# Optimization experiments

Measured on AMD Instinct MI355X. Metric: run time of the kernel, lower is better.

The kernel has to match this reference:

```python
import jax, jax.numpy as jnp
import numpy as np

B, L, D, Y = 8, 2500, 512, 8921


def setup_inputs() -> dict:
    key = jax.random.key(0)
    k1, k2, k3, k4, k5, k6 = jax.random.split(key, 6)
    x = jax.random.normal(k1, (B, L, D), dtype=jnp.float32)
    target = jax.random.uniform(k2, (B, Y), dtype=jnp.float32)
    text_inputs = jax.random.randint(k3, (B, L), 0, 50000, dtype=jnp.int32)
    # Xavier-uniform-like init for the two [Y, D] weights
    lim = float(np.sqrt(6.0 / (Y + D)))
    U_weight = jax.random.uniform(k4, (Y, D), dtype=jnp.float32, minval=-lim, maxval=lim)
    final_weight = jax.random.uniform(k5, (Y, D), dtype=jnp.float32, minval=-lim, maxval=lim)
    final_bias = jax.random.uniform(k6, (Y,), dtype=jnp.float32, minval=-0.05, maxval=0.05)
    return {"x": x, "target": target, "text_inputs": text_inputs,
            "U_weight": U_weight, "final_weight": final_weight, "final_bias": final_bias}


def reference(x, target, text_inputs, U_weight, final_weight, final_bias):
    # att: [B, Y, L] = U.weight @ x^T
    att = jnp.einsum('yd,bld->byl', U_weight, x)
    # softmax over sequence dim
    alpha = jax.nn.softmax(att, axis=2)
    # per-label context: [B, Y, D]
    m = jnp.einsum('byl,bld->byd', alpha, x)
    # gated reduction instead of a linear layer: [B, Y]
    y = jnp.einsum('byd,yd->by', m, final_weight) + final_bias
    # BCEWithLogitsLoss (mean over all elements), numerically stable
    loss = jnp.mean(jnp.maximum(y, 0.0) - y * target + jnp.log1p(jnp.exp(-jnp.abs(y))))
    return (y, loss)
```

## Files before the change

### kernel.cpp

```cpp
#include <hip/hip_runtime.h>
#include <stdint.h>

#define B_ 8
#define L_ 2500
#define D_ 512
#define Y_ 8921
#define LP 2560
#define YP 8960
#define BY 128
#define BL 256
#define BK 32
#define NKT 16
#define NSP 10
#define NBLK (70 * B_ * NSP)
#define PERX (NBLK / 8)
#define BUF 16384

typedef float f32x4 __attribute__((ext_vector_type(4)));
typedef __bf16 bf16x8 __attribute__((ext_vector_type(8)));
typedef unsigned short u16;
typedef unsigned int u32;

__device__ __forceinline__ u32 pack2(float a, float b) {
  u32 ua = __float_as_uint(a); ua = (ua + 0x7FFFu + ((ua >> 16) & 1u)) >> 16;
  u32 ub = __float_as_uint(b); ub = (ub + 0x7FFFu + ((ub >> 16) & 1u)) >> 16;
  return ua | (ub << 16);
}

__global__ void cvt_x_kernel(const float* __restrict__ x, u16* __restrict__ xb) {
  int idx = blockIdx.x * 256 + threadIdx.x;
  int row = idx >> 6;
  int c8  = (idx & 63) << 3;
  int b = row / LP;
  int l = row - b * LP;
  uint4 o;
  if (l < L_) {
    const float* s = x + (size_t)(b * L_ + l) * D_ + c8;
    float4 f0 = *(const float4*)s;
    float4 f1 = *(const float4*)(s + 4);
    o.x = pack2(f0.x, f0.y); o.y = pack2(f0.z, f0.w);
    o.z = pack2(f1.x, f1.y); o.w = pack2(f1.z, f1.w);
  } else {
    o = make_uint4(0u, 0u, 0u, 0u);
  }
  *(uint4*)(xb + (size_t)row * D_ + c8) = o;
}

__global__ void cvt_w_kernel(const float* __restrict__ U, const float* __restrict__ Wf,
                             u16* __restrict__ Ub, u16* __restrict__ Wb) {
  int idx = blockIdx.x * 256 + threadIdx.x;
  const int half = YP * 64;
  const float* src = U; u16* dst = Ub;
  int i = idx;
  if (idx >= half) { i -= half; src = Wf; dst = Wb; }
  int row = i >> 6;
  int c8  = (i & 63) << 3;
  uint4 o;
  if (row < Y_) {
    const float* s = src + (size_t)row * D_ + c8;
    float4 f0 = *(const float4*)s;
    float4 f1 = *(const float4*)(s + 4);
    o.x = pack2(f0.x, f0.y); o.y = pack2(f0.z, f0.w);
    o.z = pack2(f1.x, f1.y); o.w = pack2(f1.z, f1.w);
  } else {
    o = make_uint4(0u, 0u, 0u, 0u);
  }
  *(uint4*)(dst + (size_t)row * D_ + c8) = o;
}

__device__ __forceinline__ void async16(const u16* g, u16* l) {
  __builtin_amdgcn_global_load_lds(
      (const __attribute__((address_space(1))) u32*)g,
      (__attribute__((address_space(3))) u32*)l, 16, 0, 0);
}

__global__ __launch_bounds__(512, 2) void fused_kernel(
    const u16* __restrict__ xb,
    const u16* __restrict__ Ub,
    const u16* __restrict__ Wb,
    float* __restrict__ part)
{
  __shared__ __align__(16) u16 sB[2 * BUF];
  __shared__ float sSt[3 * 4 * BY];

  const int t    = threadIdx.x;
  const int lane = t & 63;
  const int wv   = t >> 6;
  const int wy   = wv >> 2;
  const int wl   = wv & 3;
  const int l16  = lane & 15;
  const int q    = lane >> 4;

  const int bid = blockIdx.x;
  const int w   = (bid & 7) * PERX + (bid >> 3);
  const int yt  = w / 80;
  const int rem = w - yt * 80;
  const int b   = rem / NSP;
  const int s   = rem - b * NSP;
  const int y0  = yt * BY;
  const int l0  = s * BL;

  const int srow = t >> 2;
  const int scol = (t & 3) << 3;
  const u16* gU  = Ub + (size_t)(y0 + srow) * D_ + scol;
  const u16* gW  = Wb + (size_t)(y0 + srow) * D_ + scol;
  const u16* gX0 = xb + ((size_t)b * LP + l0 + srow) * D_ + scol;
  const u16* gX1 = gX0 + (size_t)128 * D_;

  const int offU = (wy * 64 + l16) * BK + q * 8;
  const int offX = 8192 + (wl * 64 + l16) * BK + q * 8;

  auto stage = [&](int kt, int buf) {
    u16* base = sB + buf * BUF;
    const int ko = kt * BK;
    async16(gU + ko,  base + t * 8);
    async16(gW + ko,  base + 4096 + t * 8);
    async16(gX0 + ko, base + 8192 + t * 8);
    async16(gX1 + ko, base + 12288 + t * 8);
  };

  const f32x4 z4 = {0.f, 0.f, 0.f, 0.f};
  f32x4 accA[4][4], accS[4][4];
#pragma unroll
  for (int yi = 0; yi < 4; ++yi)
#pragma unroll
    for (int xi = 0; xi < 4; ++xi) { accA[yi][xi] = z4; accS[yi][xi] = z4; }

  stage(0, 0);
#pragma unroll 1
  for (int kt = 0; kt < NKT; ++kt) {
    const int cur = kt & 1;
    if (kt + 1 < NKT) {
      stage(kt + 1, cur ^ 1);
      asm volatile("s_waitcnt vmcnt(4)" ::: "memory");
    } else {
      asm volatile("s_waitcnt vmcnt(0)" ::: "memory");
    }
    __builtin_amdgcn_s_barrier();
    asm volatile("" ::: "memory");

    const u16* bb = sB + cur * BUF;
    bf16x8 xf[4];
#pragma unroll
    for (int xi = 0; xi < 4; ++xi)
      xf[xi] = *(const bf16x8*)(const void*)(bb + offX + xi * 16 * BK);
    __builtin_amdgcn_s_setprio(1);
#pragma unroll
    for (int yi = 0; yi < 4; ++yi) {
      bf16x8 aU = *(const bf16x8*)(const void*)(bb + offU + yi * 16 * BK);
      bf16x8 aW = *(const bf16x8*)(const void*)(bb + 4096 + offU + yi * 16 * BK);
#pragma unroll
      for (int xi = 0; xi < 4; ++xi) {
        accA[yi][xi] = __builtin_amdgcn_mfma_f32_16x16x32_bf16(aU, xf[xi], accA[yi][xi], 0, 0, 0);
        accS[yi][xi] = __builtin_amdgcn_mfma_f32_16x16x32_bf16(aW, xf[xi], accS[yi][xi], 0, 0, 0);
      }
    }
    __builtin_amdgcn_s_setprio(0);
    asm volatile("" ::: "memory");
    __builtin_amdgcn_s_barrier();
  }

  float M[16], Z[16], W[16];
  const bool boundary = (l0 + BL > L_);
#pragma unroll
  for (int yi = 0; yi < 4; ++yi) {
#pragma unroll
    for (int r = 0; r < 4; ++r) {
      const int si = yi * 4 + r;
      float a[4];
#pragma unroll
      for (int xi = 0; xi < 4; ++xi) {
        float v = accA[yi][xi][r];
        a[xi] = (boundary && (l0 + wl * 64 + xi * 16 + l16 >= L_)) ? -1e30f : v;
      }
      const float mx = fmaxf(fmaxf(a[0], a[1]), fmaxf(a[2], a[3]));
      float zl = 0.f, wl_ = 0.f;
#pragma unroll
      for (int xi = 0; xi < 4; ++xi) {
        const float p = __expf(a[xi] - mx);
        zl += p;
        wl_ = fmaf(p, accS[yi][xi][r], wl_);
      }
      M[si] = mx; Z[si] = zl; W[si] = wl_;
    }
  }

#pragma unroll
  for (int si = 0; si < 16; ++si) {
    float M0 = M[si], Z0 = Z[si], W0 = W[si];
#pragma unroll
    for (int st = 1; st <= 8; st <<= 1) {
      const float Mo = __shfl_xor(M0, st);
      const float Zo = __shfl_xor(Z0, st);
      const float Wo = __shfl_xor(W0, st);
      const float mn = fmaxf(M0, Mo);
      const float sa = __expf(M0 - mn);
      const float sb = __expf(Mo - mn);
      Z0 = Z0 * sa + Zo * sb;
      W0 = W0 * sa + Wo * sb;
      M0 = mn;
    }
    M[si] = M0; Z[si] = Z0; W[si] = W0;
  }

  __syncthreads();
  if (l16 == 0) {
#pragma unroll
    for (int yi = 0; yi < 4; ++yi) {
#pragma unroll
      for (int r = 0; r < 4; ++r) {
        const int si = yi * 4 + r;
        const int yloc = wy * 64 + yi * 16 + q * 4 + r;
        sSt[wl * BY + yloc]        = M[si];
        sSt[512 + wl * BY + yloc]  = Z[si];
        sSt[1024 + wl * BY + yloc] = W[si];
      }
    }
  }
  __syncthreads();
  if (t < BY) {
    float Mm = sSt[t];
#pragma unroll
    for (int k = 1; k < 4; ++k) Mm = fmaxf(Mm, sSt[k * BY + t]);
    float Zm = 0.f, Wm = 0.f;
#pragma unroll
    for (int k = 0; k < 4; ++k) {
      const float e = __expf(sSt[k * BY + t] - Mm);
      Zm = fmaf(sSt[512 + k * BY + t], e, Zm);
      Wm = fmaf(sSt[1024 + k * BY + t], e, Wm);
    }
    float* p = part + ((size_t)(b * 70 + yt) * NSP + s) * 384;
    p[t]       = Mm;
    p[128 + t] = Zm;
    p[256 + t] = Wm;
  }
}

__global__ void combine_kernel(const float* __restrict__ part,
                               const float* __restrict__ bias,
                               const float* __restrict__ target,
                               float* __restrict__ out) {
  const int idx = blockIdx.x * 256 + threadIdx.x;
  float lpart = 0.f;
  if (idx < B_ * Y_) {
    const int b = idx / Y_;
    const int y = idx - b * Y_;
    const int yt = y >> 7, yl = y & 127;
    const float* p = part + ((size_t)(b * 70 + yt) * NSP) * 384 + yl;
    float M = -1e30f;
#pragma unroll
    for (int s2 = 0; s2 < NSP; ++s2) M = fmaxf(M, p[s2 * 384]);
    float Z = 0.f, W = 0.f;
#pragma unroll
    for (int s2 = 0; s2 < NSP; ++s2) {
      const float e = __expf(p[s2 * 384] - M);
      Z = fmaf(p[s2 * 384 + 128], e, Z);
      W = fmaf(p[s2 * 384 + 256], e, W);
    }
    const float yv = W / Z + bias[y];
    out[idx] = yv;
    const float tg = target[idx];
    lpart = fmaxf(yv, 0.f) - yv * tg + log1pf(__expf(-fabsf(yv)));
  }
  lpart += __shfl_xor(lpart, 1);  lpart += __shfl_xor(lpart, 2);
  lpart += __shfl_xor(lpart, 4);  lpart += __shfl_xor(lpart, 8);
  lpart += __shfl_xor(lpart, 16); lpart += __shfl_xor(lpart, 32);
  if ((threadIdx.x & 63) == 0)
    atomicAdd(out + (size_t)B_ * Y_, lpart * (1.0f / (B_ * Y_)));
}

extern "C" void kernel_launch(void* const* d_in, const int* in_sizes, int n_in,
                              void* d_out, int out_size, void* d_ws, size_t ws_size,
                              hipStream_t stream) {
  const float* x      = (const float*)d_in[0];
  const float* target = (const float*)d_in[1];
  const float* U      = (const float*)d_in[3];
  const float* Wf     = (const float*)d_in[4];
  const float* bias   = (const float*)d_in[5];
  float* out = (float*)d_out;

  u16* xb = (u16*)d_ws;
  u16* Ub = xb + (size_t)B_ * LP * D_;
  u16* Wb = Ub + (size_t)YP * D_;
  float* part = (float*)(Wb + (size_t)YP * D_);

  hipMemsetAsync(out + (size_t)B_ * Y_, 0, sizeof(float), stream);
  cvt_x_kernel<<<dim3((B_ * LP * 64) / 256), 256, 0, stream>>>(x, xb);
  cvt_w_kernel<<<dim3((2 * YP * 64) / 256), 256, 0, stream>>>(U, Wf, Ub, Wb);
  fused_kernel<<<dim3(NBLK), 512, 0, stream>>>(xb, Ub, Wb, part);
  combine_kernel<<<dim3((B_ * Y_ + 255) / 256), 256, 0, stream>>>(part, bias, target, out);
}
```

Baseline: 674.1 us.

## Use four-slot LDS ring with two-ahead prefetch, XOR swizzle, and split MFMA phases

Replaces the double-buffered LDS staging with a four-slot ring that prefetches two K-tiles ahead. Each iteration is split into two phases, U-MFMAs then W-MFMAs, with the async loads issued between them. An XOR swizzle on LDS columns targets bank conflicts on fragment reads. LDS use doubles to about 128KB, so launch bounds drop to one block per CU. The extra barriers and lower occupancy may offset the deeper prefetch.

```diff
diff --git a/kernel.cpp b/kernel.cpp
--- a/kernel.cpp
+++ b/kernel.cpp
@@ -14,7 +14,8 @@
 #define NSP 10
 #define NBLK (70 * B_ * NSP)
 #define PERX (NBLK / 8)
-#define BUF 16384
+#define SLOT 16384
+#define RING 4
 
 typedef float f32x4 __attribute__((ext_vector_type(4)));
 typedef __bf16 bf16x8 __attribute__((ext_vector_type(8)));
@@ -74,13 +75,13 @@
       (__attribute__((address_space(3))) u32*)l, 16, 0, 0);
 }
 
-__global__ __launch_bounds__(512, 2) void fused_kernel(
+__global__ __launch_bounds__(512, 1) void fused_kernel(
     const u16* __restrict__ xb,
     const u16* __restrict__ Ub,
     const u16* __restrict__ Wb,
     float* __restrict__ part)
 {
-  __shared__ __align__(16) u16 sB[2 * BUF];
+  __shared__ __align__(16) u16 sRing[RING * SLOT];
   __shared__ float sSt[3 * 4 * BY];
 
   const int t    = threadIdx.x;
@@ -90,6 +91,7 @@
   const int wl   = wv & 3;
   const int l16  = lane & 15;
   const int q    = lane >> 4;
+  const int swz  = ((q ^ (l16 & 3)) << 3);
 
   const int bid = blockIdx.x;
   const int w   = (bid & 7) * PERX + (bid >> 3);
@@ -101,24 +103,12 @@
   const int l0  = s * BL;
 
   const int srow = t >> 2;
-  const int scol = (t & 3) << 3;
+  const int scol = (((t & 3) ^ (srow & 3)) << 3);
   const u16* gU  = Ub + (size_t)(y0 + srow) * D_ + scol;
   const u16* gW  = Wb + (size_t)(y0 + srow) * D_ + scol;
   const u16* gX0 = xb + ((size_t)b * LP + l0 + srow) * D_ + scol;
   const u16* gX1 = gX0 + (size_t)128 * D_;
 
-  const int offU = (wy * 64 + l16) * BK + q * 8;
-  const int offX = 8192 + (wl * 64 + l16) * BK + q * 8;
-
-  auto stage = [&](int kt, int buf) {
-    u16* base = sB + buf * BUF;
-    const int ko = kt * BK;
-    async16(gU + ko,  base + t * 8);
-    async16(gW + ko,  base + 4096 + t * 8);
-    async16(gX0 + ko, base + 8192 + t * 8);
-    async16(gX1 + ko, base + 12288 + t * 8);
-  };
-
   const f32x4 z4 = {0.f, 0.f, 0.f, 0.f};
   f32x4 accA[4][4], accS[4][4];
 #pragma unroll
@@ -126,38 +116,73 @@
 #pragma unroll
     for (int xi = 0; xi < 4; ++xi) { accA[yi][xi] = z4; accS[yi][xi] = z4; }
 
-  stage(0, 0);
+  {
+    u16* s0 = sRing;            u16* s1 = sRing + SLOT;
+    async16(gU,       s0 + t * 8);          async16(gX0,      s0 + 8192 + t * 8);
+    async16(gW,       s0 + 4096 + t * 8);   async16(gX1,      s0 + 12288 + t * 8);
+    async16(gU + BK,  s1 + t * 8);          async16(gX0 + BK, s1 + 8192 + t * 8);
+    async16(gW + BK,  s1 + 4096 + t * 8);   async16(gX1 + BK, s1 + 12288 + t * 8);
+    asm volatile("s_waitcnt vmcnt(4)" ::: "memory");
+    __builtin_amdgcn_s_barrier();
+    asm volatile("" ::: "memory");
+  }
+
 #pragma unroll 1
-  for (int kt = 0; kt < NKT; ++kt) {
-    const int cur = kt & 1;
-    if (kt + 1 < NKT) {
-      stage(kt + 1, cur ^ 1);
-      asm volatile("s_waitcnt vmcnt(4)" ::: "memory");
-    } else {
-      asm volatile("s_waitcnt vmcnt(0)" ::: "memory");
-    }
-    __builtin_amdgcn_s_barrier();
-    asm volatile("" ::: "memory");
-
-    const u16* bb = sB + cur * BUF;
-    bf16x8 xf[4];
-#pragma unroll
-    for (int xi = 0; xi < 4; ++xi)
-      xf[xi] = *(const bf16x8*)(const void*)(bb + offX + xi * 16 * BK);
+  for (int ts = 0; ts < NKT; ++ts) {
+    const u16* sl = sRing + (ts & 3) * SLOT;
+    const int t2 = ts + 2;
+    u16* sp = sRing + (t2 & 3) * SLOT;
+    const int ko2 = t2 * BK;
+
+    bf16x8 uf[4], xf[4];
+#pragma unroll
+    for (int i = 0; i < 4; ++i) {
+      uf[i] = *(const bf16x8*)(const void*)(sl + (wy * 64 + i * 16 + l16) * 32 + swz);
+      xf[i] = *(const bf16x8*)(const void*)(sl + 8192 + (wl * 64 + i * 16 + l16) * 32 + swz);
+    }
+    if (t2 < NKT) {
+      async16(gU + ko2,  sp + t * 8);
+      async16(gX0 + ko2, sp + 8192 + t * 8);
+    }
+    asm volatile("" ::: "memory");
+    __builtin_amdgcn_s_barrier();
+    asm volatile("" ::: "memory");
     __builtin_amdgcn_s_setprio(1);
 #pragma unroll
-    for (int yi = 0; yi < 4; ++yi) {
-      bf16x8 aU = *(const bf16x8*)(const void*)(bb + offU + yi * 16 * BK);
-      bf16x8 aW = *(const bf16x8*)(const void*)(bb + 4096 + offU + yi * 16 * BK);
-#pragma unroll
-      for (int xi = 0; xi < 4; ++xi) {
-        accA[yi][xi] = __builtin_amdgcn_mfma_f32_16x16x32_bf16(aU, xf[xi], accA[yi][xi], 0, 0, 0);
-        accS[yi][xi] = __builtin_amdgcn_mfma_f32_16x16x32_bf16(aW, xf[xi], accS[yi][xi], 0, 0, 0);
-      }
-    }
+    for (int yi = 0; yi < 4; ++yi)
+#pragma unroll
+      for (int xi = 0; xi < 4; ++xi)
+        accA[yi][xi] = __builtin_amdgcn_mfma_f32_16x16x32_bf16(uf[yi], xf[xi], accA[yi][xi], 0, 0, 0);
     __builtin_amdgcn_s_setprio(0);
     asm volatile("" ::: "memory");
     __builtin_amdgcn_s_barrier();
+    asm volatile("" ::: "memory");
+
+    bf16x8 wf[4];
+#pragma unroll
+    for (int i = 0; i < 4; ++i)
+      wf[i] = *(const bf16x8*)(const void*)(sl + 4096 + (wy * 64 + i * 16 + l16) * 32 + swz);
+    if (t2 < NKT) {
+      async16(gW + ko2,  sp + 4096 + t * 8);
+      async16(gX1 + ko2, sp + 12288 + t * 8);
+    }
+    if (ts + 1 < NKT) {
+      if (t2 < NKT) asm volatile("s_waitcnt vmcnt(4)" ::: "memory");
+      else          asm volatile("s_waitcnt vmcnt(0)" ::: "memory");
+    }
+    asm volatile("" ::: "memory");
+    __builtin_amdgcn_s_barrier();
+    asm volatile("" ::: "memory");
+    __builtin_amdgcn_s_setprio(1);
+#pragma unroll
+    for (int yi = 0; yi < 4; ++yi)
+#pragma unroll
+      for (int xi = 0; xi < 4; ++xi)
+        accS[yi][xi] = __builtin_amdgcn_mfma_f32_16x16x32_bf16(wf[yi], xf[xi], accS[yi][xi], 0, 0, 0);
+    __builtin_amdgcn_s_setprio(0);
+    asm volatile("" ::: "memory");
+    __builtin_amdgcn_s_barrier();
+    asm volatile("" ::: "memory");
   }
 
   float M[16], Z[16], W[16];
```

Result: faster. 643.8 us (-4.5%).
